# Optimization experiments

Measured on AMD Instinct MI355X. Metric: run time of the kernel, lower is better.

The kernel has to match this reference:

```python
import math
import jax, jax.numpy as jnp
import numpy as np

B, T, H = 4, 2048, 1024
E, K, F = 8, 2, 2048
CAP_FACTOR = 1.25


def setup_inputs() -> dict:
    key = jax.random.key(0)
    k1, k2, k3, k4 = jax.random.split(key, 4)
    x = jax.random.normal(k1, (B, T, H), dtype=jnp.float32)
    Wg = jax.random.normal(k2, (H, E), dtype=jnp.float32) * 0.02
    W_in = jax.random.normal(k3, (E, H, 2 * F), dtype=jnp.float32) * (1.0 / math.sqrt(H))
    W_out = jax.random.normal(k4, (E, F, H), dtype=jnp.float32) * (1.0 / math.sqrt(F))
    return {"x": x, "Wg": Wg, "W_in": W_in, "W_out": W_out}


def _moe_forward(x, Wg, W_in, W_out):
    b, t, h = x.shape
    xf = x.reshape(-1, h)                      # [S, H] flattened tokens
    S = xf.shape[0]
    C = int(math.ceil(K * S / E * CAP_FACTOR))  # per-expert capacity (drop_tokens=True)

    # --- gating (noiseless top-k, eval/RSample-off path) ---
    logits = xf @ Wg                           # [S, E]
    probs = jax.nn.softmax(logits, axis=-1)
    top_vals, top_idx = jax.lax.top_k(probs, K)  # [S, K]

    # --- capacity-ordered locations, slot-major priority (slot0 before slot1) ---
    flat_idx = top_idx.T.reshape(-1)           # [K*S], slot-major
    onehot = jax.nn.one_hot(flat_idx, E, dtype=jnp.int32)
    cum = jnp.cumsum(onehot, axis=0) - 1       # position within each expert
    loc = jnp.take_along_axis(cum, flat_idx[:, None], axis=1)[:, 0]
    loc = loc.reshape(K, S).T                  # [S, K]
    keep = loc < C                             # token-drop mask

    # --- gate weights normalized over kept slots (DeepSpeed top-k normalization) ---
    gates = top_vals * keep.astype(top_vals.dtype)       # [S, K]
    denom = jnp.maximum(gates.sum(-1, keepdims=True), 1e-9)
    gates = gates / denom

    # --- dispatch: scatter tokens into [E, C, H] buffers (pad slot C for drops) ---
    loc_c = jnp.where(keep, loc, C)
    e_flat = top_idx.reshape(-1)               # [S*K]
    l_flat = loc_c.reshape(-1)
    xk = jnp.broadcast_to(xf[:, None, :], (S, K, h)).reshape(-1, h)
    xk = jnp.where(keep.reshape(-1, 1), xk, 0.0)
    buf = jnp.zeros((E, C + 1, h), x.dtype).at[e_flat, l_flat].set(xk)
    inp = buf[:, :C]                           # [E, C, H]

    # --- GLU experts as grouped GEMMs ---
    hid = jnp.einsum('ech,ehf->ecf', inp, W_in)          # [E, C, 2F]
    a, g = jnp.split(hid, 2, axis=-1)
    hid = jax.nn.gelu(a, approximate=False) * g          # torch gelu = exact erf
    out_e = jnp.einsum('ecf,efh->ech', hid, W_out)       # [E, C, H]

    # --- combine: gather per-slot expert outputs, weight by gates, sum over k ---
    out_pad = jnp.concatenate([out_e, jnp.zeros((E, 1, h), out_e.dtype)], axis=1)
    gathered = out_pad[e_flat, l_flat].reshape(S, K, h)
    y = (gathered * gates[..., None]).sum(axis=1)        # [S, H]
    return y.reshape(b, t, h)


def reference(x, Wg, W_in, W_out):
    return _moe_forward(x, Wg, W_in, W_out)
```

## Files before the change

kernel.cpp:

```cpp
#include <hip/hip_runtime.h>
#include <hip/hip_bf16.h>
#include <math.h>

#define S_TOK 8192
#define HDIM  1024
#define FDIM  2048
#define CAP   2560

typedef unsigned short u16;
typedef short  s16x8 __attribute__((ext_vector_type(8)));
typedef float  f32x4 __attribute__((ext_vector_type(4)));

__device__ __forceinline__ u16 f2b(float f){
  unsigned u = __builtin_bit_cast(unsigned, f);
  u = (u + 0x7FFFu + ((u >> 16) & 1u)) >> 16;
  return (u16)u;
}
__device__ __forceinline__ float b2f(u16 h){
  unsigned u = ((unsigned)h) << 16;
  return __builtin_bit_cast(float, u);
}
__device__ __forceinline__ void gl_lds16(const u16* g, u16* l){
  auto gp = (const __attribute__((address_space(1))) unsigned int*)g;
  auto lp = (__attribute__((address_space(3))) unsigned int*)l;
  __builtin_amdgcn_global_load_lds(gp, lp, 16, 0, 0);
}
__device__ __forceinline__ float gelu_t(float a){
  float z = 0.7978845608f * a * (1.f + 0.044715f * a * a);
  float e = __expf(-2.f * fabsf(z));
  float th = (1.f - e) / (1.f + e);
  th = (z < 0.f) ? -th : th;
  return 0.5f * a * (1.f + th);
}

__device__ __forceinline__ int glu_reorder(int c){
  int h = (c >= 2048) ? 1 : 0;
  int cc = c - (h << 11);
  return ((cc >> 5) << 6) + (h << 5) + (cc & 31);
}

template<int REORDER>
__global__ __launch_bounds__(256) void k_transpose(const float* __restrict__ in,
                                                   u16* __restrict__ out, int R, int Cc){
  __shared__ float tl[64][65];
  int e = blockIdx.z;
  const float* ip = in + (size_t)e * R * Cc;
  u16* op = out + (size_t)e * R * Cc;
  int c0 = blockIdx.x * 64, r0 = blockIdx.y * 64;
  int t = threadIdx.x;
  int tx = t & 15, ty = t >> 4;
  #pragma unroll
  for (int p = 0; p < 4; p++){
    int r = ty + p * 16;
    float4 v = *(const float4*)&ip[(size_t)(r0 + r) * Cc + c0 + tx * 4];
    tl[r][tx * 4 + 0] = v.x; tl[r][tx * 4 + 1] = v.y;
    tl[r][tx * 4 + 2] = v.z; tl[r][tx * 4 + 3] = v.w;
  }
  __syncthreads();
  #pragma unroll
  for (int p = 0; p < 4; p++){
    int cc = ty + p * 16;
    int c = c0 + cc;
    int rp = REORDER ? glu_reorder(c) : c;
    int rr = tx * 4;
    ushort4 o;
    o.x = f2b(tl[rr + 0][cc]); o.y = f2b(tl[rr + 1][cc]);
    o.z = f2b(tl[rr + 2][cc]); o.w = f2b(tl[rr + 3][cc]);
    *(ushort4*)&op[(size_t)rp * R + r0 + rr] = o;
  }
}

__global__ __launch_bounds__(256) void k_gating(const float* __restrict__ x,
                                                const float* __restrict__ Wg,
                                                int* __restrict__ eidx, float* __restrict__ vals){
  int t = threadIdx.x, wid = t >> 6, l = t & 63;
  int s = blockIdx.x * 4 + wid;
  const float4* xr = (const float4*)(x + (size_t)s * HDIM);
  const float4* wg = (const float4*)Wg;
  double acc[8] = {0,0,0,0,0,0,0,0};
  #pragma unroll
  for (int j4 = 0; j4 < 4; j4++){
    float4 xv = xr[l * 4 + j4];
    float xa[4] = {xv.x, xv.y, xv.z, xv.w};
    #pragma unroll
    for (int q = 0; q < 4; q++){
      int h = l * 16 + j4 * 4 + q;
      float4 w0 = wg[h * 2], w1 = wg[h * 2 + 1];
      double xd = (double)xa[q];
      acc[0] += xd * w0.x; acc[1] += xd * w0.y; acc[2] += xd * w0.z; acc[3] += xd * w0.w;
      acc[4] += xd * w1.x; acc[5] += xd * w1.y; acc[6] += xd * w1.z; acc[7] += xd * w1.w;
    }
  }
  #pragma unroll
  for (int off = 32; off; off >>= 1)
    #pragma unroll
    for (int e = 0; e < 8; e++) acc[e] += __shfl_down(acc[e], off);
  if (l == 0){
    double mx = acc[0];
    #pragma unroll
    for (int e = 1; e < 8; e++) mx = acc[e] > mx ? acc[e] : mx;
    double ex[8], sum = 0.0;
    #pragma unroll
    for (int e = 0; e < 8; e++){ ex[e] = exp(acc[e] - mx); sum += ex[e]; }
    double inv = 1.0 / sum;
    double p0 = -1.0; int e0 = 0;
    #pragma unroll
    for (int e = 0; e < 8; e++){ double p = ex[e] * inv; if (p > p0){ p0 = p; e0 = e; } }
    double p1 = -1.0; int e1 = 0;
    #pragma unroll
    for (int e = 0; e < 8; e++){ double p = ex[e] * inv; if (e != e0 && p > p1){ p1 = p; e1 = e; } }
    eidx[s] = e0;          vals[s] = (float)p0;
    eidx[S_TOK + s] = e1;  vals[S_TOK + s] = (float)p1;
  }
}

__global__ __launch_bounds__(1024) void k_scan(const int* __restrict__ eidx,
                                               const float* __restrict__ vals,
                                               int* __restrict__ slot, float* __restrict__ gates,
                                               int* __restrict__ cnt){
  __shared__ int wavetot[16][9];
  __shared__ int waveoff[16][9];
  __shared__ unsigned char keepb[2 * S_TOK];
  int t = threadIdx.x, w = t >> 6, l = t & 63;
  int le[16];
  int c[8] = {0,0,0,0,0,0,0,0};
  #pragma unroll
  for (int j = 0; j < 16; j++){ int e = eidx[t * 16 + j]; le[j] = e; c[e]++; }
  int inc[8];
  #pragma unroll
  for (int e = 0; e < 8; e++) inc[e] = c[e];
  #pragma unroll
  for (int off = 1; off < 64; off <<= 1)
    #pragma unroll
    for (int e = 0; e < 8; e++){
      int v = __shfl_up(inc[e], off);
      if (l >= off) inc[e] += v;
    }
  if (l == 63)
    #pragma unroll
    for (int e = 0; e < 8; e++) wavetot[w][e] = inc[e];
  __syncthreads();
  if (t < 8){
    int run = 0;
    for (int ww = 0; ww < 16; ww++){ waveoff[ww][t] = run; run += wavetot[ww][t]; }
    cnt[t] = min(run, CAP);
  }
  __syncthreads();
  int run[8];
  #pragma unroll
  for (int e = 0; e < 8; e++) run[e] = waveoff[w][e] + (inc[e] - c[e]);
  #pragma unroll
  for (int j = 0; j < 16; j++){
    int i = t * 16 + j; int e = le[j]; int loc = run[e]++;
    int kp = (loc < CAP);
    keepb[i] = (unsigned char)kp;
    slot[i] = kp ? (e * CAP + loc) : -1;
  }
  __syncthreads();
  #pragma unroll
  for (int r = 0; r < 8; r++){
    int s = t + 1024 * r;
    float g0 = keepb[s]         ? vals[s]         : 0.f;
    float g1 = keepb[S_TOK + s] ? vals[S_TOK + s] : 0.f;
    float inv = 1.f / fmaxf(g0 + g1, 1e-9f);
    gates[s] = g0 * inv;
    gates[S_TOK + s] = g1 * inv;
  }
}

__global__ __launch_bounds__(256) void k_scatter(const float* __restrict__ x,
                                                 const int* __restrict__ slot,
                                                 u16* __restrict__ A){
  int i = blockIdx.x;
  int sl = slot[i];
  if (sl < 0) return;
  int s = i & (S_TOK - 1);
  int t = threadIdx.x;
  float4 v = ((const float4*)(x + (size_t)s * HDIM))[t];
  ushort4 o; o.x = f2b(v.x); o.y = f2b(v.y); o.z = f2b(v.z); o.w = f2b(v.w);
  ((ushort4*)(A + (size_t)sl * HDIM))[t] = o;
}


#define STAGE_A(h, tt, par) { \
    const u16* gp_ = Ap + (size_t)((h)*128 + c0*8) * LDK + (size_t)(tt) * 64 + srow_off; \
    u16* lp_ = lds + (par)*16384 + (h)*8192 + c0*512; \
    gl_lds16(gp_, lp_); gl_lds16(gp_ + (size_t)8*LDK, lp_ + 512); }

#define STAGE_B(h, tt, par) { \
    const u16* gp_ = Bp + (size_t)((h)*128 + c0*8) * LDK + (size_t)(tt) * 64 + srow_off; \
    u16* lp_ = lds + 32768 + (par)*16384 + (h)*8192 + c0*512; \
    gl_lds16(gp_, lp_); gl_lds16(gp_ + (size_t)8*LDK, lp_ + 512); }

#define CFENCE asm volatile("" ::: "memory");

#define PH(P, KSW, NH, STAGE_CODE, TAILWAIT, POST_CODE) { \
    if ((NH) == 0) { \
      _Pragma("unroll") \
      for (int m_ = 0; m_ < 8; ++m_) \
        af[m_] = *(const s16x8*)&lds[(P)*16384 + aoff + m_*1024 + (KSW)]; \
    } \
    bf[0] = *(const s16x8*)&lds[32768 + (P)*16384 + boff + (2*(NH))*1024 + (KSW)]; \
    bf[1] = *(const s16x8*)&lds[32768 + (P)*16384 + boff + (2*(NH)+1)*1024 + (KSW)]; \
    STAGE_CODE \
    CFENCE __builtin_amdgcn_s_barrier(); CFENCE \
    __builtin_amdgcn_s_setprio(1); \
    _Pragma("unroll") \
    for (int m_ = 0; m_ < 8; ++m_){ \
      acc[m_][2*(NH)]   = __builtin_amdgcn_mfma_f32_16x16x32_bf16(af[m_], bf[0], acc[m_][2*(NH)],   0, 0, 0); \
      acc[m_][2*(NH)+1] = __builtin_amdgcn_mfma_f32_16x16x32_bf16(af[m_], bf[1], acc[m_][2*(NH)+1], 0, 0, 0); \
    } \
    __builtin_amdgcn_s_setprio(0); \
    if (TAILWAIT){ asm volatile("s_waitcnt lgkmcnt(0)" ::: "memory"); } \
    POST_CODE \
    CFENCE __builtin_amdgcn_s_barrier(); CFENCE }

template<int NK, int LDK, int NB, int IS_GLU>
__global__ __launch_bounds__(512, 2) void k_gemm8(const u16* __restrict__ Aall,
                                                  const u16* __restrict__ Ball,
                                                  u16* __restrict__ Out,
                                                  const int* __restrict__ cnt){
  const int gx = gridDim.x, gy = gridDim.y;
  const int o = blockIdx.x + gx * (blockIdx.y + gy * blockIdx.z);
  const int nwg = gx * gy * (int)gridDim.z;
  const int q = nwg >> 3;
  const int w = (o & 7) * q + (o >> 3);
  const int mt = w % gx;
  const int t1 = w / gx;
  const int nt = t1 % gy;
  const int e  = t1 / gy;
  if (mt * 256 >= cnt[e]) return;
  __shared__ __align__(1024) u16 lds[65536];
  const u16* Ap = Aall + (size_t)e * CAP * LDK + (size_t)mt * 256 * LDK;
  const u16* Bp = Ball + (size_t)e * NB * LDK + (size_t)nt * 256 * LDK;

  const int t = threadIdx.x, wid = t >> 6, l = t & 63;
  const int wm = wid >> 2, wn = wid & 3;
  const int lrow = l & 15, lkhi = l >> 4;
  const int c0 = wid * 2;
  const size_t srow_off = (size_t)(l >> 3) * LDK + (size_t)(((l & 7) * 8) ^ ((l >> 3) * 8));
  const int aoff = wm * 8192 + lrow * 64;
  const int boff = (wn >> 1) * 8192 + ((wn & 1) * 64 + lrow) * 64;
  const int sx   = (l & 7) * 8;
  const int ksw0 = (lkhi * 8) ^ sx;
  const int ksw1 = (32 + lkhi * 8) ^ sx;

  f32x4 acc[8][4] = {};
  s16x8 af[8], bf[2];

  STAGE_A(0, 0, 0) STAGE_A(1, 0, 0) STAGE_B(0, 0, 0) STAGE_B(1, 0, 0)
  STAGE_A(0, 1, 1) STAGE_A(1, 1, 1)
  asm volatile("s_waitcnt vmcnt(4)" ::: "memory");
  CFENCE __builtin_amdgcn_s_barrier(); CFENCE

  #pragma unroll 1
  for (int t2 = 0; t2 < NK / 2; ++t2){
    const int te = 2 * t2;
    const bool nl = (t2 < NK / 2 - 1);
    PH(0, ksw0, 0, { STAGE_B(0, te + 1, 1) }, 0, {})
    PH(0, ksw0, 1, { STAGE_B(1, te + 1, 1) }, 0, {})
    PH(0, ksw1, 0, {}, 1, {})
    PH(0, ksw1, 1,
       { if (nl){ STAGE_A(0, te + 2, 0) STAGE_A(1, te + 2, 0) } },
       1,
       { if (nl){ asm volatile("s_waitcnt vmcnt(4)" ::: "memory"); }
         else   { asm volatile("s_waitcnt vmcnt(0)" ::: "memory"); } })
    PH(1, ksw0, 0, { if (nl){ STAGE_B(0, te + 2, 0) } }, 0, {})
    PH(1, ksw0, 1, { if (nl){ STAGE_B(1, te + 2, 0) } }, 0, {})
    PH(1, ksw1, 0, {}, 1, {})
    PH(1, ksw1, 1,
       { if (nl){ STAGE_A(0, te + 3, 1) STAGE_A(1, te + 3, 1) } },
       1,
       { if (nl){ asm volatile("s_waitcnt vmcnt(4)" ::: "memory"); } })
  }

  const int rowb = mt * 256 + wm * 128 + lkhi * 4;
  if (IS_GLU){
    u16* hp = Out + (size_t)e * CAP * FDIM;
    const int colb = (nt * 4 + wn) * 32 + lrow;
    #pragma unroll
    for (int m = 0; m < 8; ++m)
      #pragma unroll
      for (int np = 0; np < 2; ++np)
        #pragma unroll
        for (int r = 0; r < 4; ++r){
          size_t row = (size_t)(rowb + m * 16 + r);
          float a = acc[m][np][r], g = acc[m][np + 2][r];
          hp[row * FDIM + colb + np * 16] = f2b(gelu_t(a) * g);
        }
  } else {
    u16* op = Out + (size_t)e * CAP * HDIM;
    const int colb = nt * 256 + wn * 64 + lrow;
    #pragma unroll
    for (int m = 0; m < 8; ++m)
      #pragma unroll
      for (int n = 0; n < 4; ++n)
        #pragma unroll
        for (int r = 0; r < 4; ++r){
          size_t row = (size_t)(rowb + m * 16 + r);
          op[row * HDIM + colb + n * 16] = f2b(acc[m][n][r]);
        }
  }
}

__global__ __launch_bounds__(256) void k_gather(const u16* __restrict__ oute,
                                                const int* __restrict__ slot,
                                                const float* __restrict__ gates,
                                                float* __restrict__ y){
  int s = blockIdx.x, t = threadIdx.x;
  int s0 = slot[s], s1 = slot[S_TOK + s];
  float g0 = gates[s], g1 = gates[S_TOK + s];
  float4 r; r.x = r.y = r.z = r.w = 0.f;
  if (s0 >= 0){
    ushort4 v = ((const ushort4*)(oute + (size_t)s0 * HDIM))[t];
    r.x += g0 * b2f(v.x); r.y += g0 * b2f(v.y); r.z += g0 * b2f(v.z); r.w += g0 * b2f(v.w);
  }
  if (s1 >= 0){
    ushort4 v = ((const ushort4*)(oute + (size_t)s1 * HDIM))[t];
    r.x += g1 * b2f(v.x); r.y += g1 * b2f(v.y); r.z += g1 * b2f(v.z); r.w += g1 * b2f(v.w);
  }
  ((float4*)(y + (size_t)s * HDIM))[t] = r;
}

extern "C" void kernel_launch(void* const* d_in, const int* in_sizes, int n_in,
                              void* d_out, int out_size, void* d_ws, size_t ws_size,
                              hipStream_t stream){
  (void)in_sizes; (void)n_in; (void)out_size; (void)ws_size;
  const float* x     = (const float*)d_in[0];
  const float* Wg    = (const float*)d_in[1];
  const float* W_in  = (const float*)d_in[2];
  const float* W_out = (const float*)d_in[3];
  float* y = (float*)d_out;

  char* ws = (char*)d_ws;
  u16* WiT   = (u16*)(ws);
  u16* WoT   = (u16*)(ws + 67108864);
  u16* Ainp  = (u16*)(ws + 100663296);
  u16* hid   = (u16*)(ws + 142606336);
  int*   eidx  = (int*)  (ws + 226492416);
  float* vals  = (float*)(ws + 226492416 + 65536);
  int*   slot  = (int*)  (ws + 226492416 + 131072);
  float* gates = (float*)(ws + 226492416 + 196608);
  int*   cnt   = (int*)  (ws + 226492416 + 262144);

  k_transpose<1><<<dim3(64, 16, 8), dim3(256), 0, stream>>>(W_in,  WiT, 1024, 4096);
  k_transpose<0><<<dim3(16, 32, 8), dim3(256), 0, stream>>>(W_out, WoT, 2048, 1024);
  k_gating   <<<dim3(2048), dim3(256),  0, stream>>>(x, Wg, eidx, vals);
  k_scan     <<<dim3(1),    dim3(1024), 0, stream>>>(eidx, vals, slot, gates, cnt);
  k_scatter  <<<dim3(2 * S_TOK), dim3(256), 0, stream>>>(x, slot, Ainp);
  k_gemm8<16, 1024, 4096, 1><<<dim3(10, 16, 8), dim3(512), 0, stream>>>(Ainp, WiT, hid, cnt);
  k_gemm8<32, 2048, 1024, 0><<<dim3(10, 4, 8),  dim3(512), 0, stream>>>(hid, WoT, Ainp, cnt);
  k_gather   <<<dim3(S_TOK), dim3(256), 0, stream>>>(Ainp, slot, gates, y);
}
```

Baseline: 616.6 us.

## Fuse fp32 weight transpose and bf16 conversion into GEMM B-operand staging

Removes the two separate weight transpose/convert kernels. Each expert GEMM now loads fp32 W_in/W_out tiles straight from global memory into registers, packs them to bf16 with v_cvt_pk_bf16_f32, and writes them into swizzled LDS. The GLU column reorder moves into per-thread column offsets. This drops a full pass over 96MB of fp32 weights and the bf16 copy, in exchange for reading twice the bytes per B tile inside the GEMM, repeated across M tiles, and more register pressure and VALU work in the pipelined loop.

```diff
diff --git a/kernel.cpp b/kernel.cpp
--- a/kernel.cpp
+++ b/kernel.cpp
@@ -24,6 +24,14 @@
   auto gp = (const __attribute__((address_space(1))) unsigned int*)g;
   auto lp = (__attribute__((address_space(3))) unsigned int*)l;
   __builtin_amdgcn_global_load_lds(gp, lp, 16, 0, 0);
+}
+__device__ __forceinline__ unsigned pkbf(float a, float b){
+  unsigned d;
+  asm("v_cvt_pk_bf16_f32 %0, %1, %2" : "=v"(d) : "v"(a), "v"(b));
+  return d;
+}
+__device__ __forceinline__ float f4get(const float4& v, int i){
+  return ((const float*)&v)[i];
 }
 __device__ __forceinline__ float gelu_t(float a){
   float z = 0.7978845608f * a * (1.f + 0.044715f * a * a);
@@ -31,43 +39,6 @@
   float th = (1.f - e) / (1.f + e);
   th = (z < 0.f) ? -th : th;
   return 0.5f * a * (1.f + th);
-}
-
-__device__ __forceinline__ int glu_reorder(int c){
-  int h = (c >= 2048) ? 1 : 0;
-  int cc = c - (h << 11);
-  return ((cc >> 5) << 6) + (h << 5) + (cc & 31);
-}
-
-template<int REORDER>
-__global__ __launch_bounds__(256) void k_transpose(const float* __restrict__ in,
-                                                   u16* __restrict__ out, int R, int Cc){
-  __shared__ float tl[64][65];
-  int e = blockIdx.z;
-  const float* ip = in + (size_t)e * R * Cc;
-  u16* op = out + (size_t)e * R * Cc;
-  int c0 = blockIdx.x * 64, r0 = blockIdx.y * 64;
-  int t = threadIdx.x;
-  int tx = t & 15, ty = t >> 4;
-  #pragma unroll
-  for (int p = 0; p < 4; p++){
-    int r = ty + p * 16;
-    float4 v = *(const float4*)&ip[(size_t)(r0 + r) * Cc + c0 + tx * 4];
-    tl[r][tx * 4 + 0] = v.x; tl[r][tx * 4 + 1] = v.y;
-    tl[r][tx * 4 + 2] = v.z; tl[r][tx * 4 + 3] = v.w;
-  }
-  __syncthreads();
-  #pragma unroll
-  for (int p = 0; p < 4; p++){
-    int cc = ty + p * 16;
-    int c = c0 + cc;
-    int rp = REORDER ? glu_reorder(c) : c;
-    int rr = tx * 4;
-    ushort4 o;
-    o.x = f2b(tl[rr + 0][cc]); o.y = f2b(tl[rr + 1][cc]);
-    o.z = f2b(tl[rr + 2][cc]); o.w = f2b(tl[rr + 3][cc]);
-    *(ushort4*)&op[(size_t)rp * R + r0 + rr] = o;
-  }
 }
 
 __global__ __launch_bounds__(256) void k_gating(const float* __restrict__ x,
@@ -187,14 +158,29 @@
     u16* lp_ = lds + (par)*16384 + (h)*8192 + c0*512; \
     gl_lds16(gp_, lp_); gl_lds16(gp_ + (size_t)8*LDK, lp_ + 512); }
 
-#define STAGE_B(h, tt, par) { \
-    const u16* gp_ = Bp + (size_t)((h)*128 + c0*8) * LDK + (size_t)(tt) * 64 + srow_off; \
-    u16* lp_ = lds + 32768 + (par)*16384 + (h)*8192 + c0*512; \
-    gl_lds16(gp_, lp_); gl_lds16(gp_ + (size_t)8*LDK, lp_ + 512); }
+#define LOADB(R, h, tt) { \
+    const float* gp_ = Bsrc_e + (size_t)((tt)*64 + kl) * NSRC + colh[h]; \
+    R[0] = *(const float4*)gp_;             R[1] = *(const float4*)(gp_ + NSRC); \
+    R[2] = *(const float4*)(gp_ + 2*NSRC);  R[3] = *(const float4*)(gp_ + 3*NSRC); }
+
+#define WRITEB(R, h, par) { \
+    _Pragma("unroll") \
+    for (int i_ = 0; i_ < 4; ++i_){ \
+      int row_ = (h)*128 + nl0 + i_; \
+      int ad_  = 32768 + (par)*16384 + row_*64 + (kl ^ ((row_ & 7) * 8)); \
+      uint2 d_; \
+      d_.x = pkbf(f4get(R[0], i_), f4get(R[1], i_)); \
+      d_.y = pkbf(f4get(R[2], i_), f4get(R[3], i_)); \
+      *(uint2*)&lds[ad_] = d_; \
+    } }
 
 #define CFENCE asm volatile("" ::: "memory");
-
-#define PH(P, KSW, NH, STAGE_CODE, TAILWAIT, POST_CODE) { \
+#define VM8 asm volatile("s_waitcnt vmcnt(8)" ::: "memory");
+#define VM4 asm volatile("s_waitcnt vmcnt(4)" ::: "memory");
+#define VM0 asm volatile("s_waitcnt vmcnt(0)" ::: "memory");
+#define LGKM0 asm volatile("s_waitcnt lgkmcnt(0)" ::: "memory");
+
+#define PHASE(P, KSW, NH, PRE, POST) { \
     if ((NH) == 0) { \
       _Pragma("unroll") \
       for (int m_ = 0; m_ < 8; ++m_) \
@@ -202,7 +188,7 @@
     } \
     bf[0] = *(const s16x8*)&lds[32768 + (P)*16384 + boff + (2*(NH))*1024 + (KSW)]; \
     bf[1] = *(const s16x8*)&lds[32768 + (P)*16384 + boff + (2*(NH)+1)*1024 + (KSW)]; \
-    STAGE_CODE \
+    PRE \
     CFENCE __builtin_amdgcn_s_barrier(); CFENCE \
     __builtin_amdgcn_s_setprio(1); \
     _Pragma("unroll") \
@@ -211,13 +197,12 @@
       acc[m_][2*(NH)+1] = __builtin_amdgcn_mfma_f32_16x16x32_bf16(af[m_], bf[1], acc[m_][2*(NH)+1], 0, 0, 0); \
     } \
     __builtin_amdgcn_s_setprio(0); \
-    if (TAILWAIT){ asm volatile("s_waitcnt lgkmcnt(0)" ::: "memory"); } \
-    POST_CODE \
+    POST \
     CFENCE __builtin_amdgcn_s_barrier(); CFENCE }
 
-template<int NK, int LDK, int NB, int IS_GLU>
+template<int NK, int LDK, int NSRC, int IS_GLU>
 __global__ __launch_bounds__(512, 2) void k_gemm8(const u16* __restrict__ Aall,
-                                                  const u16* __restrict__ Ball,
+                                                  const float* __restrict__ Bsrc,
                                                   u16* __restrict__ Out,
                                                   const int* __restrict__ cnt){
   const int gx = gridDim.x, gy = gridDim.y;
@@ -231,8 +216,8 @@
   const int e  = t1 / gy;
   if (mt * 256 >= cnt[e]) return;
   __shared__ __align__(1024) u16 lds[65536];
-  const u16* Ap = Aall + (size_t)e * CAP * LDK + (size_t)mt * 256 * LDK;
-  const u16* Bp = Ball + (size_t)e * NB * LDK + (size_t)nt * 256 * LDK;
+  const u16*   Ap     = Aall + (size_t)e * CAP * LDK + (size_t)mt * 256 * LDK;
+  const float* Bsrc_e = Bsrc + (size_t)e * LDK * NSRC;
 
   const int t = threadIdx.x, wid = t >> 6, l = t & 63;
   const int wm = wid >> 2, wn = wid & 3;
@@ -245,33 +230,56 @@
   const int ksw0 = (lkhi * 8) ^ sx;
   const int ksw1 = (32 + lkhi * 8) ^ sx;
 
+  const int kh  = wid & 1;
+  const int nb  = wid >> 1;
+  const int kl  = kh * 32 + (l & 7) * 4;
+  const int nl0 = nb * 32 + (l >> 3) * 4;
+  int colh[2];
+  #pragma unroll
+  for (int h = 0; h < 2; ++h){
+    int rpg = nt * 256 + h * 128 + nl0;
+    colh[h] = IS_GLU ? (((rpg >> 5) & 1) * 2048 + ((rpg >> 6) << 5) + (rpg & 31)) : rpg;
+  }
+
   f32x4 acc[8][4] = {};
   s16x8 af[8], bf[2];
-
-  STAGE_A(0, 0, 0) STAGE_A(1, 0, 0) STAGE_B(0, 0, 0) STAGE_B(1, 0, 0)
+  float4 b0r[4], b1r[4];
+
+  LOADB(b0r, 0, 0)
+  LOADB(b1r, 1, 0)
+  STAGE_A(0, 0, 0) STAGE_A(1, 0, 0)
+  VM8
+  WRITEB(b0r, 0, 0)
+  LOADB(b0r, 0, 1)
+  VM8
+  WRITEB(b1r, 1, 0)
+  LOADB(b1r, 1, 1)
+  VM8
   STAGE_A(0, 1, 1) STAGE_A(1, 1, 1)
-  asm volatile("s_waitcnt vmcnt(4)" ::: "memory");
+  LGKM0
   CFENCE __builtin_amdgcn_s_barrier(); CFENCE
 
   #pragma unroll 1
   for (int t2 = 0; t2 < NK / 2; ++t2){
     const int te = 2 * t2;
     const bool nl = (t2 < NK / 2 - 1);
-    PH(0, ksw0, 0, { STAGE_B(0, te + 1, 1) }, 0, {})
-    PH(0, ksw0, 1, { STAGE_B(1, te + 1, 1) }, 0, {})
-    PH(0, ksw1, 0, {}, 1, {})
-    PH(0, ksw1, 1,
-       { if (nl){ STAGE_A(0, te + 2, 0) STAGE_A(1, te + 2, 0) } },
-       1,
-       { if (nl){ asm volatile("s_waitcnt vmcnt(4)" ::: "memory"); }
-         else   { asm volatile("s_waitcnt vmcnt(0)" ::: "memory"); } })
-    PH(1, ksw0, 0, { if (nl){ STAGE_B(0, te + 2, 0) } }, 0, {})
-    PH(1, ksw0, 1, { if (nl){ STAGE_B(1, te + 2, 0) } }, 0, {})
-    PH(1, ksw1, 0, {}, 1, {})
-    PH(1, ksw1, 1,
-       { if (nl){ STAGE_A(0, te + 3, 1) STAGE_A(1, te + 3, 1) } },
-       1,
-       { if (nl){ asm volatile("s_waitcnt vmcnt(4)" ::: "memory"); } })
+    PHASE(0, ksw0, 0,
+      { VM8 WRITEB(b0r, 0, 1) if (nl){ LOADB(b0r, 0, te + 2) } }, {})
+    PHASE(0, ksw0, 1,
+      { if (nl){ VM8 } else { VM4 } WRITEB(b1r, 1, 1) if (nl){ LOADB(b1r, 1, te + 2) } }, {})
+    PHASE(0, ksw1, 0, {}, { LGKM0 })
+    PHASE(0, ksw1, 1, {},
+      { LGKM0
+        if (nl){ VM8 STAGE_A(0, te + 2, 0) STAGE_A(1, te + 2, 0) }
+        else   { VM0 } })
+    PHASE(1, ksw0, 0,
+      { if (nl){ VM8 WRITEB(b0r, 0, 0) LOADB(b0r, 0, te + 3) } }, {})
+    PHASE(1, ksw0, 1,
+      { if (nl){ VM8 WRITEB(b1r, 1, 0) LOADB(b1r, 1, te + 3) } }, {})
+    PHASE(1, ksw1, 0, {}, { LGKM0 })
+    PHASE(1, ksw1, 1, {},
+      { LGKM0
+        if (nl){ VM8 STAGE_A(0, te + 3, 1) STAGE_A(1, te + 3, 1) } })
   }
 
   const int rowb = mt * 256 + wm * 128 + lkhi * 4;
@@ -333,22 +341,18 @@
   float* y = (float*)d_out;
 
   char* ws = (char*)d_ws;
-  u16* WiT   = (u16*)(ws);
-  u16* WoT   = (u16*)(ws + 67108864);
-  u16* Ainp  = (u16*)(ws + 100663296);
-  u16* hid   = (u16*)(ws + 142606336);
-  int*   eidx  = (int*)  (ws + 226492416);
-  float* vals  = (float*)(ws + 226492416 + 65536);
-  int*   slot  = (int*)  (ws + 226492416 + 131072);
-  float* gates = (float*)(ws + 226492416 + 196608);
-  int*   cnt   = (int*)  (ws + 226492416 + 262144);
-
-  k_transpose<1><<<dim3(64, 16, 8), dim3(256), 0, stream>>>(W_in,  WiT, 1024, 4096);
-  k_transpose<0><<<dim3(16, 32, 8), dim3(256), 0, stream>>>(W_out, WoT, 2048, 1024);
+  u16* Ainp  = (u16*)(ws);
+  u16* hid   = (u16*)(ws + 41943040);
+  int*   eidx  = (int*)  (ws + 125829120);
+  float* vals  = (float*)(ws + 125829120 + 65536);
+  int*   slot  = (int*)  (ws + 125829120 + 131072);
+  float* gates = (float*)(ws + 125829120 + 196608);
+  int*   cnt   = (int*)  (ws + 125829120 + 262144);
+
   k_gating   <<<dim3(2048), dim3(256),  0, stream>>>(x, Wg, eidx, vals);
   k_scan     <<<dim3(1),    dim3(1024), 0, stream>>>(eidx, vals, slot, gates, cnt);
   k_scatter  <<<dim3(2 * S_TOK), dim3(256), 0, stream>>>(x, slot, Ainp);
-  k_gemm8<16, 1024, 4096, 1><<<dim3(10, 16, 8), dim3(512), 0, stream>>>(Ainp, WiT, hid, cnt);
-  k_gemm8<32, 2048, 1024, 0><<<dim3(10, 4, 8),  dim3(512), 0, stream>>>(hid, WoT, Ainp, cnt);
+  k_gemm8<16, 1024, 4096, 1><<<dim3(10, 16, 8), dim3(512), 0, stream>>>(Ainp, W_in, hid, cnt);
+  k_gemm8<32, 2048, 1024, 0><<<dim3(10, 4, 8),  dim3(512), 0, stream>>>(hid, W_out, Ainp, cnt);
   k_gather   <<<dim3(S_TOK), dim3(256), 0, stream>>>(Ainp, slot, gates, y);
 }
```

Measured after the change: 1.048 ms. +70.0%, slower.
